# Optimization experiments

Measured on AMD Instinct MI355X. Metric: run time of the kernel, lower is better.

Reference implementation:

```python
import jax, jax.numpy as jnp
import numpy as np

B, N, F, H = 1, 8192, 512, 64
NEG_BIAS = -9.0  # GAT adjacency bias for non-edges


def setup_inputs() -> dict:
    key = jax.random.key(0)
    ks = jax.random.split(key, 6)
    features = jax.random.normal(ks[0], (B, N, F), dtype=jnp.float32)
    edge = jax.random.uniform(ks[1], (B, N, N)) < 0.02
    bias_mat = jnp.where(edge, 0.0, NEG_BIAS).astype(jnp.float32)
    W = jax.random.normal(ks[2], (F, H), dtype=jnp.float32) * 0.05   # 1x1 conv, no bias
    a1 = jax.random.normal(ks[3], (H, 1), dtype=jnp.float32) * 0.05  # f_1 1x1 conv
    b1 = jnp.zeros((1,), dtype=jnp.float32)
    a2 = jax.random.normal(ks[4], (H, 1), dtype=jnp.float32) * 0.05  # f_2 1x1 conv
    b2 = jnp.zeros((1,), dtype=jnp.float32)
    return {"features": features, "bias_mat": bias_mat, "W": W,
            "a1": a1, "b1": b1, "a2": a2, "b2": b2}


def reference(features, bias_mat, W, a1, b1, a2, b2):
    # 1x1 conv projection (no bias): [B,N,F] @ [F,H] -> [B,N,H]
    fts = jnp.einsum('bnf,fh->bnh', features, W)
    # per-node scalar attention terms: [B,N,1]
    f1 = jnp.einsum('bnh,ho->bno', fts, a1) + b1
    f2 = jnp.einsum('bnh,ho->bno', fts, a2) + b2
    # additive pairwise logits: [B,N,N]
    logits = f1 + jnp.swapaxes(f2, 1, 2)
    # masked softmax over neighbors, then (as written in source) add bias again
    coefs = jax.nn.softmax(jax.nn.relu(logits) + bias_mat, axis=-1) + bias_mat
    # weighted aggregation: [B,N,N] @ [B,N,H] -> [B,N,H]
    vals = jnp.einsum('bmn,bnh->bmh', coefs, fts)
    return jax.nn.elu(vals)
```

## Files before the change

kernel.cpp:

```cpp
#include <hip/hip_runtime.h>
#include <math.h>

#define N 8192
#define FDIM 512
#define H 64
#define MAXE 512

__global__ __launch_bounds__(256) void k_fts(const float* __restrict__ feat,
                                             const float* __restrict__ W,
                                             float* __restrict__ fts,
                                             float* __restrict__ T) {
    __shared__ float Af[64][65];
    __shared__ float Bf[64][64];
    __shared__ float colred[16][64];
    int t = threadIdx.x;
    int row0 = blockIdx.x * 64;
    int hq = (t & 15) * 4;
    int rq = (t >> 4) * 4;
    float acc[4][4] = {};
    for (int k0 = 0; k0 < FDIM; k0 += 64) {
#pragma unroll
        for (int i = 0; i < 4; ++i) {
            int l = t + i * 256;
            int r = l >> 4;
            int c4 = (l & 15) * 4;
            float4 av = *(const float4*)&feat[(size_t)(row0 + r) * FDIM + k0 + c4];
            Af[r][c4 + 0] = av.x; Af[r][c4 + 1] = av.y;
            Af[r][c4 + 2] = av.z; Af[r][c4 + 3] = av.w;
            float4 bv = *(const float4*)&W[(size_t)(k0 + r) * H + c4];
            *(float4*)&Bf[r][c4] = bv;
        }
        __syncthreads();
#pragma unroll 8
        for (int kk = 0; kk < 64; ++kk) {
            float a[4];
#pragma unroll
            for (int j = 0; j < 4; ++j) a[j] = Af[rq + j][kk];
            float4 b = *(const float4*)&Bf[kk][hq];
#pragma unroll
            for (int j = 0; j < 4; ++j) {
                acc[j][0] += a[j] * b.x;
                acc[j][1] += a[j] * b.y;
                acc[j][2] += a[j] * b.z;
                acc[j][3] += a[j] * b.w;
            }
        }
        __syncthreads();
    }
#pragma unroll
    for (int j = 0; j < 4; ++j) {
        float4 v = make_float4(acc[j][0], acc[j][1], acc[j][2], acc[j][3]);
        *(float4*)&fts[(size_t)(row0 + rq + j) * H + hq] = v;
    }
#pragma unroll
    for (int i = 0; i < 4; ++i)
        colred[t >> 4][hq + i] = acc[0][i] + acc[1][i] + acc[2][i] + acc[3][i];
    __syncthreads();
    if (t < H) {
        float s = 0.f;
#pragma unroll
        for (int g = 0; g < 16; ++g) s += colred[g][t];
        atomicAdd(&T[t], s);
    }
}

__global__ __launch_bounds__(256) void k_f12(const float* __restrict__ fts,
                                             const float* __restrict__ a1, const float* __restrict__ b1,
                                             const float* __restrict__ a2, const float* __restrict__ b2,
                                             float* __restrict__ f1, float* __restrict__ f2) {
    int t = threadIdx.x;
    int lane = t & 63;
    int m = blockIdx.x * 4 + (t >> 6);
    float v = fts[(size_t)m * H + lane];
    float s1 = v * a1[lane];
    float s2 = v * a2[lane];
#pragma unroll
    for (int o = 32; o; o >>= 1) { s1 += __shfl_xor(s1, o); s2 += __shfl_xor(s2, o); }
    if (lane == 0) { f1[m] = s1 + b1[0]; f2[m] = s2 + b2[0]; }
}

__global__ __launch_bounds__(256) void k_main(const float* __restrict__ bias,
                                              const float* __restrict__ fts,
                                              const float* __restrict__ f1g,
                                              const float* __restrict__ f2g,
                                              const float* __restrict__ T,
                                              float* __restrict__ out) {
    __shared__ int   listN[MAXE];
    __shared__ float listF[MAXE];
    __shared__ float redW[8][64];
    __shared__ float redF[8][64];
    __shared__ float redE[8];
    __shared__ int s_cnt;
    const int t = threadIdx.x;
    const int m = blockIdx.x;
    const int lane = t & 63;
    const int w = t >> 6;
    if (t == 0) s_cnt = 0;
    __syncthreads();
    const float f1m = f1g[m];

    const float4* brow = (const float4*)(bias + (size_t)m * N);
    float4 r[8];
#pragma unroll
    for (int i = 0; i < 8; ++i) r[i] = brow[t + i * 256];
    const unsigned long long lmask = (1ULL << lane) - 1ULL;
#pragma unroll
    for (int i = 0; i < 8; ++i) {
        int nb = (t + i * 256) * 4;
        float c0 = r[i].x, c1 = r[i].y, c2 = r[i].z, c3 = r[i].w;
#pragma unroll
        for (int q = 0; q < 4; ++q) {
            float cv = q == 0 ? c0 : q == 1 ? c1 : q == 2 ? c2 : c3;
            bool is_edge = (cv == 0.f);
            unsigned long long mb = __ballot(is_edge);
            int base = 0;
            if (lane == 0) base = atomicAdd(&s_cnt, (int)__popcll(mb));
            base = __shfl(base, 0);
            if (is_edge) {
                int idx = base + (int)__popcll(mb & lmask);
                if (idx < MAXE) listN[idx] = nb + q;
            }
        }
    }
    __syncthreads();
    const int cnt = s_cnt < MAXE ? s_cnt : MAXE;
    for (int j = t; j < cnt; j += 256) listF[j] = f2g[listN[j]];
    __syncthreads();

    const int sub = lane >> 5;
    const int hh = (lane & 31) * 2;
    const int slot = w * 2 + sub;
    float aWx = 0.f, aWy = 0.f, aFx = 0.f, aFy = 0.f, aE = 0.f;
    int e = slot;
    float ff0 = 0.f; float2 v0 = make_float2(0.f, 0.f);
    if (e < cnt) { ff0 = listF[e]; v0 = *(const float2*)&fts[(size_t)listN[e] * H + hh]; }
    while (e < cnt) {
        int e1 = e + 8;
        float ff1 = 0.f; float2 v1 = make_float2(0.f, 0.f);
        if (e1 < cnt) { ff1 = listF[e1]; v1 = *(const float2*)&fts[(size_t)listN[e1] * H + hh]; }
        float ee = __expf(fmaxf(f1m + ff0, 0.f));
        aWx += ee * v0.x; aWy += ee * v0.y;
        aFx += v0.x;      aFy += v0.y;
        aE += ee;
        ff0 = ff1; v0 = v1; e = e1;
    }
    redW[slot][hh] = aWx; redW[slot][hh + 1] = aWy;
    redF[slot][hh] = aFx; redF[slot][hh + 1] = aFy;
    if ((lane & 31) == 0) redE[slot] = aE;
    __syncthreads();

    if (t < H) {
        float eW = 0.f, eF = 0.f, eE = 0.f;
#pragma unroll
        for (int s = 0; s < 8; ++s) { eW += redW[s][t]; eF += redF[s][t]; eE += redE[s]; }
        float S = (cnt > 0) ? eW / eE : 0.f;
        float val = S - 9.0f * (T[t] - eF);
        out[(size_t)m * H + t] = val > 0.f ? val : expm1f(val);
    }
}

extern "C" void kernel_launch(void* const* d_in, const int* in_sizes, int n_in,
                              void* d_out, int out_size, void* d_ws, size_t ws_size,
                              hipStream_t stream) {
    const float* feat = (const float*)d_in[0];
    const float* bias = (const float*)d_in[1];
    const float* W    = (const float*)d_in[2];
    const float* a1   = (const float*)d_in[3];
    const float* b1   = (const float*)d_in[4];
    const float* a2   = (const float*)d_in[5];
    const float* b2   = (const float*)d_in[6];
    float* out = (float*)d_out;

    float* ws   = (float*)d_ws;
    float* fts  = ws;
    float* f1   = fts + (size_t)N * H;
    float* f2   = f1 + N;
    float* T    = f2 + N;

    hipMemsetAsync(T, 0, H * sizeof(float), stream);
    hipLaunchKernelGGL(k_fts,  dim3(N / 64), dim3(256), 0, stream, feat, W, fts, T);
    hipLaunchKernelGGL(k_f12,  dim3(N / 4),  dim3(256), 0, stream, fts, a1, b1, a2, b2, f1, f2);
    hipLaunchKernelGGL(k_main, dim3(N), dim3(256), 0, stream, bias, fts, f1, f2, T, out);
}
```

Measured before the change: 419.7 us.

## Fuse f1/f2 projection into GEMM, prefix-scan edge compaction, wider gather

Folds the per-node attention dot products into the projection GEMM epilogue using shuffle reductions, which removes a separate kernel launch and a re-read of fts. The GEMM tile is halved to 32 rows so twice as many blocks run. In the main kernel, the per-element ballot plus shared atomic compaction is replaced by a per-thread count and a wave/block prefix scan that writes edges in order. The neighbor gather now uses 16 groups with float4 loads and reads f2 directly instead of staging it in shared memory. The main kernel is dominated by streaming the 256MB bias matrix, so the gains are likely limited.

After: 401.0 us. -4.5%, faster.

```diff
diff --git a/kernel.cpp b/kernel.cpp
--- a/kernel.cpp
+++ b/kernel.cpp
@@ -8,53 +8,74 @@
 
 __global__ __launch_bounds__(256) void k_fts(const float* __restrict__ feat,
                                              const float* __restrict__ W,
+                                             const float* __restrict__ a1v,
+                                             const float* __restrict__ b1v,
+                                             const float* __restrict__ a2v,
+                                             const float* __restrict__ b2v,
                                              float* __restrict__ fts,
+                                             float* __restrict__ f1,
+                                             float* __restrict__ f2,
                                              float* __restrict__ T) {
-    __shared__ float Af[64][65];
+    __shared__ float Af[32][65];
     __shared__ float Bf[64][64];
     __shared__ float colred[16][64];
-    int t = threadIdx.x;
-    int row0 = blockIdx.x * 64;
-    int hq = (t & 15) * 4;
-    int rq = (t >> 4) * 4;
-    float acc[4][4] = {};
+    const int t = threadIdx.x;
+    const int row0 = blockIdx.x * 32;
+    const int hq = (t & 15) * 4;
+    const int rq = (t >> 4) * 2;
+    float acc[2][4] = {};
     for (int k0 = 0; k0 < FDIM; k0 += 64) {
 #pragma unroll
-        for (int i = 0; i < 4; ++i) {
+        for (int i = 0; i < 2; ++i) {
             int l = t + i * 256;
             int r = l >> 4;
             int c4 = (l & 15) * 4;
             float4 av = *(const float4*)&feat[(size_t)(row0 + r) * FDIM + k0 + c4];
             Af[r][c4 + 0] = av.x; Af[r][c4 + 1] = av.y;
             Af[r][c4 + 2] = av.z; Af[r][c4 + 3] = av.w;
-            float4 bv = *(const float4*)&W[(size_t)(k0 + r) * H + c4];
-            *(float4*)&Bf[r][c4] = bv;
+        }
+#pragma unroll
+        for (int i = 0; i < 4; ++i) {
+            int l = t + i * 256;
+            int r = l >> 4;
+            int c4 = (l & 15) * 4;
+            *(float4*)&Bf[r][c4] = *(const float4*)&W[(size_t)(k0 + r) * H + c4];
         }
         __syncthreads();
 #pragma unroll 8
         for (int kk = 0; kk < 64; ++kk) {
-            float a[4];
-#pragma unroll
-            for (int j = 0; j < 4; ++j) a[j] = Af[rq + j][kk];
+            float a0 = Af[rq][kk];
+            float a1_ = Af[rq + 1][kk];
             float4 b = *(const float4*)&Bf[kk][hq];
-#pragma unroll
-            for (int j = 0; j < 4; ++j) {
-                acc[j][0] += a[j] * b.x;
-                acc[j][1] += a[j] * b.y;
-                acc[j][2] += a[j] * b.z;
-                acc[j][3] += a[j] * b.w;
-            }
+            acc[0][0] += a0 * b.x;  acc[0][1] += a0 * b.y;
+            acc[0][2] += a0 * b.z;  acc[0][3] += a0 * b.w;
+            acc[1][0] += a1_ * b.x; acc[1][1] += a1_ * b.y;
+            acc[1][2] += a1_ * b.z; acc[1][3] += a1_ * b.w;
         }
         __syncthreads();
     }
 #pragma unroll
-    for (int j = 0; j < 4; ++j) {
+    for (int j = 0; j < 2; ++j) {
         float4 v = make_float4(acc[j][0], acc[j][1], acc[j][2], acc[j][3]);
         *(float4*)&fts[(size_t)(row0 + rq + j) * H + hq] = v;
     }
+    float pa1[4], pa2[4];
+#pragma unroll
+    for (int i = 0; i < 4; ++i) { pa1[i] = a1v[hq + i]; pa2[i] = a2v[hq + i]; }
+#pragma unroll
+    for (int j = 0; j < 2; ++j) {
+        float s1 = acc[j][0] * pa1[0] + acc[j][1] * pa1[1] + acc[j][2] * pa1[2] + acc[j][3] * pa1[3];
+        float s2 = acc[j][0] * pa2[0] + acc[j][1] * pa2[1] + acc[j][2] * pa2[2] + acc[j][3] * pa2[3];
+#pragma unroll
+        for (int o = 8; o; o >>= 1) { s1 += __shfl_xor(s1, o); s2 += __shfl_xor(s2, o); }
+        if ((t & 15) == 0) {
+            f1[row0 + rq + j] = s1 + b1v[0];
+            f2[row0 + rq + j] = s2 + b2v[0];
+        }
+    }
 #pragma unroll
     for (int i = 0; i < 4; ++i)
-        colred[t >> 4][hq + i] = acc[0][i] + acc[1][i] + acc[2][i] + acc[3][i];
+        colred[t >> 4][hq + i] = acc[0][i] + acc[1][i];
     __syncthreads();
     if (t < H) {
         float s = 0.f;
@@ -62,21 +83,6 @@
         for (int g = 0; g < 16; ++g) s += colred[g][t];
         atomicAdd(&T[t], s);
     }
-}
-
-__global__ __launch_bounds__(256) void k_f12(const float* __restrict__ fts,
-                                             const float* __restrict__ a1, const float* __restrict__ b1,
-                                             const float* __restrict__ a2, const float* __restrict__ b2,
-                                             float* __restrict__ f1, float* __restrict__ f2) {
-    int t = threadIdx.x;
-    int lane = t & 63;
-    int m = blockIdx.x * 4 + (t >> 6);
-    float v = fts[(size_t)m * H + lane];
-    float s1 = v * a1[lane];
-    float s2 = v * a2[lane];
-#pragma unroll
-    for (int o = 32; o; o >>= 1) { s1 += __shfl_xor(s1, o); s2 += __shfl_xor(s2, o); }
-    if (lane == 0) { f1[m] = s1 + b1[0]; f2[m] = s2 + b2[0]; }
 }
 
 __global__ __launch_bounds__(256) void k_main(const float* __restrict__ bias,
@@ -86,73 +92,86 @@
                                               const float* __restrict__ T,
                                               float* __restrict__ out) {
     __shared__ int   listN[MAXE];
-    __shared__ float listF[MAXE];
-    __shared__ float redW[8][64];
-    __shared__ float redF[8][64];
-    __shared__ float redE[8];
+    __shared__ float redW[16][64];
+    __shared__ float redF[16][64];
+    __shared__ float redE[16];
+    __shared__ int wbase[4];
     __shared__ int s_cnt;
     const int t = threadIdx.x;
     const int m = blockIdx.x;
     const int lane = t & 63;
     const int w = t >> 6;
-    if (t == 0) s_cnt = 0;
-    __syncthreads();
     const float f1m = f1g[m];
 
     const float4* brow = (const float4*)(bias + (size_t)m * N);
     float4 r[8];
 #pragma unroll
     for (int i = 0; i < 8; ++i) r[i] = brow[t + i * 256];
-    const unsigned long long lmask = (1ULL << lane) - 1ULL;
+    int c = 0;
+#pragma unroll
+    for (int i = 0; i < 8; ++i)
+        c += (r[i].x == 0.f) + (r[i].y == 0.f) + (r[i].z == 0.f) + (r[i].w == 0.f);
+    int sc = c;
+#pragma unroll
+    for (int o = 1; o < 64; o <<= 1) {
+        int u = __shfl_up(sc, o);
+        if (lane >= o) sc += u;
+    }
+    if (lane == 63) wbase[w] = sc;
+    __syncthreads();
+    int base = 0;
+#pragma unroll
+    for (int ww = 0; ww < 4; ++ww) if (ww < w) base += wbase[ww];
+    int pos = base + sc - c;
 #pragma unroll
     for (int i = 0; i < 8; ++i) {
         int nb = (t + i * 256) * 4;
-        float c0 = r[i].x, c1 = r[i].y, c2 = r[i].z, c3 = r[i].w;
-#pragma unroll
-        for (int q = 0; q < 4; ++q) {
-            float cv = q == 0 ? c0 : q == 1 ? c1 : q == 2 ? c2 : c3;
-            bool is_edge = (cv == 0.f);
-            unsigned long long mb = __ballot(is_edge);
-            int base = 0;
-            if (lane == 0) base = atomicAdd(&s_cnt, (int)__popcll(mb));
-            base = __shfl(base, 0);
-            if (is_edge) {
-                int idx = base + (int)__popcll(mb & lmask);
-                if (idx < MAXE) listN[idx] = nb + q;
-            }
-        }
-    }
+        if (r[i].x == 0.f) { if (pos < MAXE) listN[pos] = nb;     ++pos; }
+        if (r[i].y == 0.f) { if (pos < MAXE) listN[pos] = nb + 1; ++pos; }
+        if (r[i].z == 0.f) { if (pos < MAXE) listN[pos] = nb + 2; ++pos; }
+        if (r[i].w == 0.f) { if (pos < MAXE) listN[pos] = nb + 3; ++pos; }
+    }
+    if (t == 255) s_cnt = pos;
     __syncthreads();
     const int cnt = s_cnt < MAXE ? s_cnt : MAXE;
-    for (int j = t; j < cnt; j += 256) listF[j] = f2g[listN[j]];
-    __syncthreads();
-
-    const int sub = lane >> 5;
-    const int hh = (lane & 31) * 2;
-    const int slot = w * 2 + sub;
-    float aWx = 0.f, aWy = 0.f, aFx = 0.f, aFy = 0.f, aE = 0.f;
-    int e = slot;
-    float ff0 = 0.f; float2 v0 = make_float2(0.f, 0.f);
-    if (e < cnt) { ff0 = listF[e]; v0 = *(const float2*)&fts[(size_t)listN[e] * H + hh]; }
+
+    const int g = t >> 4;
+    const int h4 = (t & 15) * 4;
+    float4 aW = make_float4(0.f, 0.f, 0.f, 0.f);
+    float4 aF = make_float4(0.f, 0.f, 0.f, 0.f);
+    float aE = 0.f;
+    int e = g;
+    float4 v0 = make_float4(0.f, 0.f, 0.f, 0.f);
+    float ff0 = 0.f;
+    if (e < cnt) {
+        int n = listN[e];
+        v0 = *(const float4*)&fts[(size_t)n * H + h4];
+        ff0 = f2g[n];
+    }
     while (e < cnt) {
-        int e1 = e + 8;
-        float ff1 = 0.f; float2 v1 = make_float2(0.f, 0.f);
-        if (e1 < cnt) { ff1 = listF[e1]; v1 = *(const float2*)&fts[(size_t)listN[e1] * H + hh]; }
+        int e1 = e + 16;
+        float4 v1 = make_float4(0.f, 0.f, 0.f, 0.f);
+        float ff1 = 0.f;
+        if (e1 < cnt) {
+            int n1 = listN[e1];
+            v1 = *(const float4*)&fts[(size_t)n1 * H + h4];
+            ff1 = f2g[n1];
+        }
         float ee = __expf(fmaxf(f1m + ff0, 0.f));
-        aWx += ee * v0.x; aWy += ee * v0.y;
-        aFx += v0.x;      aFy += v0.y;
+        aW.x += ee * v0.x; aW.y += ee * v0.y; aW.z += ee * v0.z; aW.w += ee * v0.w;
+        aF.x += v0.x;      aF.y += v0.y;      aF.z += v0.z;      aF.w += v0.w;
         aE += ee;
-        ff0 = ff1; v0 = v1; e = e1;
-    }
-    redW[slot][hh] = aWx; redW[slot][hh + 1] = aWy;
-    redF[slot][hh] = aFx; redF[slot][hh + 1] = aFy;
-    if ((lane & 31) == 0) redE[slot] = aE;
+        v0 = v1; ff0 = ff1; e = e1;
+    }
+    *(float4*)&redW[g][h4] = aW;
+    *(float4*)&redF[g][h4] = aF;
+    if ((t & 15) == 0) redE[g] = aE;
     __syncthreads();
 
     if (t < H) {
         float eW = 0.f, eF = 0.f, eE = 0.f;
 #pragma unroll
-        for (int s = 0; s < 8; ++s) { eW += redW[s][t]; eF += redF[s][t]; eE += redE[s]; }
+        for (int s = 0; s < 16; ++s) { eW += redW[s][t]; eF += redF[s][t]; eE += redE[s]; }
         float S = (cnt > 0) ? eW / eE : 0.f;
         float val = S - 9.0f * (T[t] - eF);
         out[(size_t)m * H + t] = val > 0.f ? val : expm1f(val);
@@ -171,14 +190,15 @@
     const float* b2   = (const float*)d_in[6];
     float* out = (float*)d_out;
 
-    float* ws   = (float*)d_ws;
-    float* fts  = ws;
-    float* f1   = fts + (size_t)N * H;
-    float* f2   = f1 + N;
-    float* T    = f2 + N;
+    float* ws  = (float*)d_ws;
+    float* fts = ws;
+    float* f1  = fts + (size_t)N * H;
+    float* f2  = f1 + N;
+    float* T   = f2 + N;
 
     hipMemsetAsync(T, 0, H * sizeof(float), stream);
-    hipLaunchKernelGGL(k_fts,  dim3(N / 64), dim3(256), 0, stream, feat, W, fts, T);
-    hipLaunchKernelGGL(k_f12,  dim3(N / 4),  dim3(256), 0, stream, fts, a1, b1, a2, b2, f1, f2);
-    hipLaunchKernelGGL(k_main, dim3(N), dim3(256), 0, stream, bias, fts, f1, f2, T, out);
+    hipLaunchKernelGGL(k_fts,  dim3(N / 32), dim3(256), 0, stream,
+                       feat, W, a1, b1, a2, b2, fts, f1, f2, T);
+    hipLaunchKernelGGL(k_main, dim3(N), dim3(256), 0, stream,
+                       bias, fts, f1, f2, T, out);
 }
```
